# Kernel optimization log

Hardware: AMD Instinct MI355X
Metric: run time of the kernel (lower is better)

The kernel has to match this reference:

```python
import jax, jax.numpy as jnp
import numpy as np

D_MODEL = 512
NUM_HEADS = 8
PROJ_DIM = 64
SEQ_LEN = 2048
BATCH = 16
CHUNK = (SEQ_LEN + PROJ_DIM - 1) // PROJ_DIM  # 32
FILTER_HEIGHTS = (1, 3, 5)


def build_cluster_table(S, P):
    """table[R-1, c, :] = indices of positions assigned to cluster c when R real tokens, padded with R."""
    C = (S + P - 1) // P
    table = np.zeros((S, P, C), dtype=np.int32)
    cs = np.arange(P)
    for R in range(1, S + 1):
        assign = np.minimum(np.arange(R) * P // R, P - 1)  # nondecreasing
        starts = np.searchsorted(assign, cs, side='left')
        ends = np.searchsorted(assign, cs, side='right')
        row = np.full((P, C), R, dtype=np.int32)
        for c in range(P):
            n = ends[c] - starts[c]
            row[c, :n] = np.arange(starts[c], ends[c], dtype=np.int32)
        table[R - 1] = row
    return table


def setup_inputs() -> dict:
    key = jax.random.key(0)
    ks = jax.random.split(key, 16)
    glorot = lambda k, shape: jax.random.normal(k, shape, jnp.float32) * np.sqrt(2.0 / (shape[-2] + shape[-1]))
    inp = {
        'x': jax.random.normal(ks[0], (BATCH, SEQ_LEN, D_MODEL), jnp.float32),
        'mask': jnp.ones((BATCH, SEQ_LEN), dtype=bool),
        'wq': glorot(ks[1], (D_MODEL, D_MODEL)),
        'wk': glorot(ks[2], (D_MODEL, D_MODEL)),
        'wv': glorot(ks[3], (D_MODEL, D_MODEL)),
        'EW': glorot(ks[4], (NUM_HEADS, PROJ_DIM, CHUNK)),
        'FW': glorot(ks[5], (NUM_HEADS, PROJ_DIM, CHUNK)),
        'conv_w1': jax.random.normal(ks[6], (1, PROJ_DIM, 1, 1), jnp.float32) * 0.05,
        'conv_w3': jax.random.normal(ks[7], (3, PROJ_DIM, 1, 1), jnp.float32) * 0.05,
        'conv_w5': jax.random.normal(ks[8], (5, PROJ_DIM, 1, 1), jnp.float32) * 0.05,
        'conv_b': jnp.zeros((3,), jnp.float32),
        'dense_w': glorot(ks[9], (D_MODEL, D_MODEL)),
        'dense_b': jnp.zeros((D_MODEL,), jnp.float32),
        'cluster_table': jnp.asarray(build_cluster_table(SEQ_LEN, PROJ_DIM)),
    }
    return inp


def _conv_same(x, w):
    # x: [N, S, P, 1] NHWC ; w: [h, P, 1, 1] HWIO ; 'SAME' padding, stride 1
    return jax.lax.conv_general_dilated(
        x, w, window_strides=(1, 1), padding='SAME',
        dimension_numbers=('NHWC', 'HWIO', 'NHWC'))


def reference(x, mask, wq, wk, wv, EW, FW, conv_w1, conv_w3, conv_w5, conv_b,
              dense_w, dense_b, cluster_table):
    B, S, D = x.shape
    H, P, C = EW.shape
    depth = D // H

    q = x @ wq
    k = x @ wk
    v = x @ wv
    split = lambda t: t.reshape(B, S, H, depth).transpose(0, 2, 1, 3)  # [B,H,S,d]
    q, k0, v0 = split(q), split(k), split(v)

    # pad one extra (zero) position at index S for padded cluster slots
    kp = jnp.pad(k0, ((0, 0), (0, 0), (0, 1), (0, 0)))
    vp = jnp.pad(v0, ((0, 0), (0, 0), (0, 1), (0, 0)))

    counts = jnp.clip(mask.astype(jnp.int32).sum(axis=1), 1, S)
    pos = cluster_table[counts - 1]  # [B, P, C] int32

    # per-batch gather of K/V cluster chunks: [B,H,P,C,d]
    gather = lambda kv_b, pos_b: kv_b[:, pos_b, :]
    k_chunks = jax.vmap(gather)(kp, pos)
    v_chunks = jax.vmap(gather)(vp, pos)

    # clustered Linformer projections (c=proj_dim, l=chunk)
    k_proj = jnp.einsum('bhcld,hcl->bhcd', k_chunks, EW)  # [B,H,P,d]
    v_proj = jnp.einsum('bhcld,hcl->bhcd', v_chunks, FW)

    scale = 1.0 / jnp.sqrt(jnp.asarray(depth, jnp.float32))
    scores = jnp.einsum('bhsd,bhrd->bhsr', q, k_proj) * scale  # [B,H,S,P]

    # multi-kernel conv fusion over attention scores
    s4 = scores.reshape(B * H, S, P, 1)
    outs = jnp.stack([
        _conv_same(s4, conv_w1) + conv_b[0],
        _conv_same(s4, conv_w3) + conv_b[1],
        _conv_same(s4, conv_w5) + conv_b[2],
    ], axis=-1)  # [BH,S,P,1,3]
    scores = jnp.mean(outs, axis=-1)[..., 0].reshape(B, H, S, P)

    weights = jax.nn.softmax(scores, axis=-1)
    attn = jnp.einsum('bhsr,bhrd->bhsd', weights, v_proj)
    concat = attn.transpose(0, 2, 1, 3).reshape(B, S, D)
    return concat @ dense_w + dense_b
```

## Files before the change

kernel.cpp:

```cpp
#include <hip/hip_runtime.h>
#include <hip/hip_bf16.h>

typedef unsigned short u16;
typedef unsigned int   u32;
typedef unsigned char  u8;
typedef __attribute__((ext_vector_type(8))) __bf16 bfrag;
typedef __attribute__((ext_vector_type(4))) float  f32x4;

#define DEV __device__ __forceinline__

DEV u16 f2bf(float f){
  union { float f; u32 u; } v; v.f = f;
  u32 u = v.u;
  u32 r = (u + 0x7fffu + ((u >> 16) & 1u)) >> 16;
  return (u16)r;
}
DEV float bf2f(u16 x){
  union { u32 u; float f; } v; v.u = ((u32)x) << 16;
  return v.f;
}
DEV void gload16(const void* g, void* l){
  __builtin_amdgcn_global_load_lds((const __attribute__((address_space(1))) void*)g,
                                   (__attribute__((address_space(3))) void*)l, 16, 0, 0);
}

__global__ void k_prep(const float* __restrict__ x, const void* __restrict__ mask,
                       const float* __restrict__ wq, const float* __restrict__ wk,
                       const float* __restrict__ wv, const float* __restrict__ dw,
                       u16* __restrict__ xb, u16* __restrict__ wb, u16* __restrict__ dwb,
                       int* __restrict__ counts){
  int gb = blockIdx.x, t = threadIdx.x;
  if (gb < 16){
    int b = gb;
    u32 h0 = *(const u32*)mask;
    int mode = (h0 == 0x3f800000u) ? 2 : (h0 == 1u) ? 1 : 0;
    int cnt = 0;
    if (mode == 0){
      const u8* p = (const u8*)mask + (size_t)b * 2048;
      for (int i = t; i < 2048; i += 256) cnt += (p[i] != 0);
    } else if (mode == 1){
      const int* p = (const int*)mask + (size_t)b * 2048;
      for (int i = t; i < 2048; i += 256) cnt += (p[i] != 0);
    } else {
      const float* p = (const float*)mask + (size_t)b * 2048;
      for (int i = t; i < 2048; i += 256) cnt += (p[i] != 0.0f);
    }
    __shared__ int red[256];
    red[t] = cnt; __syncthreads();
    for (int s = 128; s > 0; s >>= 1){ if (t < s) red[t] += red[t + s]; __syncthreads(); }
    if (t == 0){ int c = red[0]; if (c < 1) c = 1; if (c > 2048) c = 2048; counts[b] = c; }
  } else if (gb < 400){
    int c = (gb - 16) * 256 + t;
    int kb8 = c / 1536, n = c % 1536;
    const float* w = (n < 512) ? wq : (n < 1024) ? wk : wv;
    int nn = n & 511;
    union { u16 o[8]; uint4 v; } u;
    #pragma unroll
    for (int j = 0; j < 8; ++j) u.o[j] = f2bf(w[(size_t)(kb8 * 8 + j) * 512 + nn]);
    *(uint4*)(wb + (size_t)c * 8) = u.v;
  } else if (gb < 528){
    int c = (gb - 400) * 256 + t;
    int kb8 = c >> 9, nn = c & 511;
    union { u16 o[8]; uint4 v; } u;
    #pragma unroll
    for (int j = 0; j < 8; ++j) u.o[j] = f2bf(dw[(size_t)(kb8 * 8 + j) * 512 + nn]);
    *(uint4*)(dwb + (size_t)c * 8) = u.v;
  } else {
    int i = (gb - 528) * 256 + t;
    int stride = (gridDim.x - 528) * 256;
    for (; i < 2097152; i += stride){
      const float4* s = (const float4*)(x + (size_t)i * 8);
      float4 a = s[0], b = s[1];
      union { u16 o[8]; uint4 v; } u;
      u.o[0]=f2bf(a.x); u.o[1]=f2bf(a.y); u.o[2]=f2bf(a.z); u.o[3]=f2bf(a.w);
      u.o[4]=f2bf(b.x); u.o[5]=f2bf(b.y); u.o[6]=f2bf(b.z); u.o[7]=f2bf(b.w);
      *(uint4*)(xb + (size_t)i * 8) = u.v;
    }
  }
}

template<int MODE>
__launch_bounds__(256, 8)
__global__ void k_gemm(const u16* __restrict__ A, const u16* __restrict__ Bp,
                       u16* __restrict__ q, u16* __restrict__ kk, u16* __restrict__ vv,
                       float* __restrict__ out, const float* __restrict__ bias,
                       int N, int nbn){
  __shared__ __align__(16) char sA[16384];
  __shared__ __align__(16) char sB[16384];
  const int tid = threadIdx.x;
  const int wid = tid >> 6, lane = tid & 63;
  int id = blockIdx.x;
  int per = gridDim.x >> 3;
  int lin = (id & 7) * per + (id >> 3);
  const int bm = lin / nbn;
  const int bn = lin - bm * nbn;
  const int wm = wid >> 1, wn = wid & 1;
  const int l15 = lane & 15, l4 = lane >> 4;

  f32x4 acc[4][4] = {};

  const char* Ab = (const char*)A;
  const char* Bb = (const char*)Bp;

  for (int kt = 0; kt < 8; ++kt){
    __syncthreads();
    #pragma unroll
    for (int t = 0; t < 4; ++t){
      int chunk = (wid * 4 + t) * 64 + lane;
      int row = chunk >> 3, slot = chunk & 7;
      const char* g = Ab + ((size_t)(bm * 128 + row) * 1024) + kt * 128 + ((slot ^ (row & 7)) << 4);
      gload16(g, sA + (wid * 4 + t) * 1024);
    }
    #pragma unroll
    for (int t = 0; t < 4; ++t){
      int idx = wid * 4 + t;
      int kb8l = idx >> 1, col = ((idx & 1) << 6) + lane;
      const char* g = Bb + ((size_t)((kt * 8 + kb8l) * N + bn * 128 + col) << 4);
      gload16(g, sB + idx * 1024);
    }
    __syncthreads();
    #pragma unroll
    for (int ks = 0; ks < 2; ++ks){
      bfrag af[4], bfv[4];
      #pragma unroll
      for (int mt = 0; mt < 4; ++mt){
        int row = wm * 64 + mt * 16 + l15;
        int slot = ks * 4 + l4;
        af[mt] = __builtin_bit_cast(bfrag, *(const uint4*)(sA + row * 128 + ((slot << 4) ^ ((row & 7) << 4))));
      }
      #pragma unroll
      for (int nt = 0; nt < 4; ++nt){
        int kb8l = ks * 4 + l4;
        int col = wn * 64 + nt * 16 + l15;
        bfv[nt] = __builtin_bit_cast(bfrag, *(const uint4*)(sB + ((kb8l * 128 + col) << 4)));
      }
      #pragma unroll
      for (int mt = 0; mt < 4; ++mt)
        #pragma unroll
        for (int nt = 0; nt < 4; ++nt)
          acc[mt][nt] = __builtin_amdgcn_mfma_f32_16x16x32_bf16(af[mt], bfv[nt], acc[mt][nt], 0, 0, 0);
    }
  }
  #pragma unroll
  for (int mt = 0; mt < 4; ++mt){
    #pragma unroll
    for (int nt = 0; nt < 4; ++nt){
      int col = bn * 128 + wn * 64 + nt * 16 + l15;
      #pragma unroll
      for (int r = 0; r < 4; ++r){
        int row = bm * 128 + wm * 64 + mt * 16 + (l4 << 2) + r;
        float val = acc[mt][nt][r];
        if (MODE == 0){
          int which = col >> 9, h = (col >> 6) & 7, dd = col & 63;
          u16* dst = (which == 0) ? q : (which == 1) ? kk : vv;
          int b = row >> 11, s = row & 2047;
          dst[(((size_t)(b * 8 + h) * 2048 + s) << 6) + dd] = f2bf(val);
        } else {
          out[(size_t)row * 512 + col] = val + bias[col];
        }
      }
    }
  }
}

__launch_bounds__(256, 2)
__global__ void k_proj(const u16* __restrict__ kg, const u16* __restrict__ vg,
                       const float* __restrict__ EW, const float* __restrict__ FW,
                       const float* __restrict__ w1, const float* __restrict__ w3,
                       const float* __restrict__ w5, const int* __restrict__ table,
                       const int* __restrict__ counts,
                       u16* __restrict__ KW, u16* __restrict__ vp){
  int bh = blockIdx.y, b = bh >> 3, h = bh & 7;
  int ddq = blockIdx.x;
  int t = threadIdx.x;
  __shared__ float Wf[5][128];
  __shared__ float kp[64][20];
  for (int w = t; w < 640; w += 256){
    int i = w >> 7, j = w & 127;
    float a = 0.f;
    if (j >= 32 && j < 96){
      int jj = j - 32;
      a = w5[i * 64 + jj];
      if (i >= 1 && i <= 3) a += w3[(i - 1) * 64 + jj];
      if (i == 2) a += w1[jj];
      a *= (1.0f / 3.0f) * 0.125f;
    }
    Wf[i][j] = a;
  }
  int cnt = counts[b];
  const int* tab = table + (size_t)(cnt - 1) * 2048;
  int c = t >> 2, sub = t & 3;
  int dd = ddq * 16 + sub * 4;
  float ka[4] = {0.f, 0.f, 0.f, 0.f}, va[4] = {0.f, 0.f, 0.f, 0.f};
  const u16* kbase = kg + ((size_t)bh << 17) + dd;
  const u16* vbase = vg + ((size_t)bh << 17) + dd;
  const float* ewr = EW + h * 2048 + c * 32;
  const float* fwr = FW + h * 2048 + c * 32;
  #pragma unroll
  for (int l0 = 0; l0 < 32; l0 += 8){
    int4 i0 = *(const int4*)(tab + c * 32 + l0);
    int4 i1 = *(const int4*)(tab + c * 32 + l0 + 4);
    int idx[8] = {i0.x, i0.y, i0.z, i0.w, i1.x, i1.y, i1.z, i1.w};
    uint2 kq[8], vq[8];
    #pragma unroll
    for (int j = 0; j < 8; ++j){
      int ic = idx[j] < 2047 ? idx[j] : 2047;
      kq[j] = *(const uint2*)(kbase + ((size_t)ic << 6));
      vq[j] = *(const uint2*)(vbase + ((size_t)ic << 6));
    }
    #pragma unroll
    for (int j = 0; j < 8; ++j){
      float valid = (idx[j] < 2048) ? 1.0f : 0.0f;
      float we = ewr[l0 + j] * valid, wf = fwr[l0 + j] * valid;
      union { uint2 u2; u16 s[4]; } ku, vu;
      ku.u2 = kq[j]; vu.u2 = vq[j];
      #pragma unroll
      for (int m = 0; m < 4; ++m){
        ka[m] += we * bf2f(ku.s[m]);
        va[m] += wf * bf2f(vu.s[m]);
      }
    }
  }
  *(float4*)(&kp[c][sub * 4]) = make_float4(ka[0], ka[1], ka[2], ka[3]);
  {
    int pg = c >> 3, pp = c & 7;
    #pragma unroll
    for (int m = 0; m < 4; ++m)
      vp[(((size_t)bh * 8 + pg) * 64 + (dd + m)) * 8 + pp] = f2bf(va[m]);
  }
  __syncthreads();
  float acc[5][4];
  #pragma unroll
  for (int i = 0; i < 5; ++i)
    #pragma unroll
    for (int m = 0; m < 4; ++m) acc[i][m] = 0.f;
  for (int u = 0; u < 64; ++u){
    float4 k4 = *(const float4*)(&kp[u][sub * 4]);
    #pragma unroll
    for (int i = 0; i < 5; ++i){
      float w = Wf[i][u - c + 63];
      acc[i][0] += w * k4.x; acc[i][1] += w * k4.y;
      acc[i][2] += w * k4.z; acc[i][3] += w * k4.w;
    }
  }
  #pragma unroll
  for (int i = 0; i < 5; ++i){
    union { u16 s[4]; uint2 u2; } o;
    #pragma unroll
    for (int m = 0; m < 4; ++m) o.s[m] = f2bf(acc[i][m]);
    *(uint2*)(KW + (((size_t)bh * 40 + i * 8 + (dd >> 3)) * 64 + c) * 8 + (dd & 7)) = o.u2;
  }
}

__launch_bounds__(256, 2)
__global__ void k_attn(const u16* __restrict__ qg, const u16* __restrict__ KWg,
                       const u16* __restrict__ vpg, u16* __restrict__ concat){
  __shared__ __align__(16) char sKW[40960];
  __shared__ __align__(16) char sVP[8192];
  __shared__ __align__(16) char sQ[8704];
  char* sW = sQ;
  int bh = blockIdx.y, b = bh >> 3, h = bh & 7;
  int tid = threadIdx.x, wid = tid >> 6, lane = tid & 63;
  int l15 = lane & 15, l4 = lane >> 4;

  const char* kwb = (const char*)KWg + (size_t)bh * 40960;
  #pragma unroll
  for (int t = 0; t < 10; ++t){
    int inst = wid * 10 + t;
    gload16(kwb + ((size_t)(inst * 64 + lane) << 4), sKW + inst * 1024);
  }
  const char* vpb = (const char*)vpg + (size_t)bh * 8192;
  #pragma unroll
  for (int t = 0; t < 2; ++t){
    int inst = wid * 2 + t;
    gload16(vpb + ((size_t)(inst * 64 + lane) << 4), sVP + inst * 1024);
  }
  const u16* qb = qg + ((size_t)bh << 17);

  for (int st = 0; st < 8; ++st){
    int s0 = ((blockIdx.x << 3) + st) << 6;
    for (int ch = tid; ch < 544; ch += 256){
      int row = ch >> 3, slot = ch & 7;
      int gr = s0 - 2 + row;
      uint4 val = make_uint4(0u, 0u, 0u, 0u);
      if (gr >= 0 && gr < 2048) val = *(const uint4*)(qb + ((size_t)gr << 6) + (slot << 3));
      *(uint4*)(sQ + row * 128 + ((slot << 4) ^ ((row & 7) << 4))) = val;
    }
    __syncthreads();

    f32x4 acc[4] = {};
    #pragma unroll
    for (int kb = 0; kb < 10; ++kb){
      int i = kb >> 1;
      int row = wid * 16 + l15 + i;
      int dd0b = ((kb & 1) << 6) + (l4 << 4);
      bfrag a = __builtin_bit_cast(bfrag, *(const uint4*)(sQ + row * 128 + (dd0b ^ ((row & 7) << 4))));
      int kb8 = kb * 4 + l4;
      #pragma unroll
      for (int nt = 0; nt < 4; ++nt){
        bfrag bv = __builtin_bit_cast(bfrag, *(const uint4*)(sKW + ((kb8 * 64 + nt * 16 + l15) << 4)));
        acc[nt] = __builtin_amdgcn_mfma_f32_16x16x32_bf16(a, bv, acc[nt], 0, 0, 0);
      }
    }
    float wgt[4][4];
    #pragma unroll
    for (int r = 0; r < 4; ++r){
      float m = fmaxf(fmaxf(acc[0][r], acc[1][r]), fmaxf(acc[2][r], acc[3][r]));
      m = fmaxf(m, __shfl_xor(m, 1));
      m = fmaxf(m, __shfl_xor(m, 2));
      m = fmaxf(m, __shfl_xor(m, 4));
      m = fmaxf(m, __shfl_xor(m, 8));
      float e0 = __expf(acc[0][r] - m), e1 = __expf(acc[1][r] - m);
      float e2 = __expf(acc[2][r] - m), e3 = __expf(acc[3][r] - m);
      float sum = e0 + e1 + e2 + e3;
      sum += __shfl_xor(sum, 1);
      sum += __shfl_xor(sum, 2);
      sum += __shfl_xor(sum, 4);
      sum += __shfl_xor(sum, 8);
      float inv = 1.0f / sum;
      wgt[0][r] = e0 * inv; wgt[1][r] = e1 * inv; wgt[2][r] = e2 * inv; wgt[3][r] = e3 * inv;
    }
    __syncthreads();
    #pragma unroll
    for (int r = 0; r < 4; ++r){
      int row = wid * 16 + (l4 << 2) + r;
      #pragma unroll
      for (int nt = 0; nt < 4; ++nt){
        int pb = (nt * 16 + l15) << 1;
        *(u16*)(sW + row * 128 + (pb ^ ((row & 7) << 4))) = f2bf(wgt[nt][r]);
      }
    }
    __syncthreads();
    f32x4 acc2[4] = {};
    #pragma unroll
    for (int ks = 0; ks < 2; ++ks){
      int row = wid * 16 + l15;
      int pb = (ks << 6) + (l4 << 4);
      bfrag a = __builtin_bit_cast(bfrag, *(const uint4*)(sW + row * 128 + (pb ^ ((row & 7) << 4))));
      int pg = ks * 4 + l4;
      #pragma unroll
      for (int nt = 0; nt < 4; ++nt){
        bfrag bv = __builtin_bit_cast(bfrag, *(const uint4*)(sVP + ((pg * 64 + nt * 16 + l15) << 4)));
        acc2[nt] = __builtin_amdgcn_mfma_f32_16x16x32_bf16(a, bv, acc2[nt], 0, 0, 0);
      }
    }
    #pragma unroll
    for (int nt = 0; nt < 4; ++nt){
      int col = (h << 6) + nt * 16 + l15;
      #pragma unroll
      for (int r = 0; r < 4; ++r){
        int s = s0 + wid * 16 + (l4 << 2) + r;
        concat[(((size_t)b << 11) + s) * 512 + col] = f2bf(acc2[nt][r]);
      }
    }
    __syncthreads();
  }
}

extern "C" void kernel_launch(void* const* d_in, const int* in_sizes, int n_in,
                              void* d_out, int out_size, void* d_ws, size_t ws_size,
                              hipStream_t stream){
  const float* x   = (const float*)d_in[0];
  const void*  mask= d_in[1];
  const float* wq  = (const float*)d_in[2];
  const float* wk  = (const float*)d_in[3];
  const float* wv  = (const float*)d_in[4];
  const float* EW  = (const float*)d_in[5];
  const float* FW  = (const float*)d_in[6];
  const float* cw1 = (const float*)d_in[7];
  const float* cw3 = (const float*)d_in[8];
  const float* cw5 = (const float*)d_in[9];
  const float* dw  = (const float*)d_in[11];
  const float* db  = (const float*)d_in[12];
  const int* table = (const int*)d_in[13];
  float* out = (float*)d_out;

  char* ws = (char*)d_ws;
  u16* xb     = (u16*)(ws);
  u16* wb     = (u16*)(ws + 33554432);
  u16* dwb    = (u16*)(ws + 35127296);
  u16* q      = (u16*)(ws + 35651584);
  u16* kk     = (u16*)(ws + 69206016);
  u16* vv     = (u16*)(ws + 102760448);
  u16* KW     = (u16*)(ws + 136314880);
  u16* vp     = (u16*)(ws + 141557760);
  int* counts = (int*)(ws + 142606336);
  u16* concat = xb;

  hipLaunchKernelGGL(k_prep, dim3(2064), dim3(256), 0, stream,
                     x, mask, wq, wk, wv, dw, xb, wb, dwb, counts);
  hipLaunchKernelGGL((k_gemm<0>), dim3(3072), dim3(256), 0, stream,
                     xb, wb, q, kk, vv, (float*)nullptr, (const float*)nullptr, 1536, 12);
  hipLaunchKernelGGL(k_proj, dim3(4, 128), dim3(256), 0, stream,
                     kk, vv, EW, FW, cw1, cw3, cw5, table, counts, KW, vp);
  hipLaunchKernelGGL(k_attn, dim3(4, 128), dim3(256), 0, stream, q, KW, vp, concat);
  hipLaunchKernelGGL((k_gemm<1>), dim3(1024), dim3(256), 0, stream,
                     concat, dwb, (u16*)nullptr, (u16*)nullptr, (u16*)nullptr, out, db, 512, 4);
}
```

Baseline: 183.3 us.

## Double-buffer Q tiles in attention kernel to prefetch next tile during compute

Splits the Q shared buffer into two ping-pong buffers plus a separate softmax-weight buffer, so the global loads for the next 64-row Q tile are issued into registers before the score MFMAs and stored to LDS after softmax. The load latency of the next tile can then hide behind the current tile's compute, and two of the four barriers per iteration are removed. The cost is more LDS per block (about 75 KB against about 57 KB before) and extra registers for the prefetched data, which could lower occupancy under the two-blocks-per-CU launch bound.

```diff
diff --git a/kernel.cpp b/kernel.cpp
--- a/kernel.cpp
+++ b/kernel.cpp
@@ -257,8 +257,9 @@
                        const u16* __restrict__ vpg, u16* __restrict__ concat){
   __shared__ __align__(16) char sKW[40960];
   __shared__ __align__(16) char sVP[8192];
-  __shared__ __align__(16) char sQ[8704];
-  char* sW = sQ;
+  __shared__ __align__(16) char sQ0[8704];
+  __shared__ __align__(16) char sQ1[8704];
+  __shared__ __align__(16) char sW[8704];
   int bh = blockIdx.y, b = bh >> 3, h = bh & 7;
   int tid = threadIdx.x, wid = tid >> 6, lane = tid & 63;
   int l15 = lane & 15, l4 = lane >> 4;
@@ -277,16 +278,37 @@
   }
   const u16* qb = qg + ((size_t)bh << 17);
 
-  for (int st = 0; st < 8; ++st){
-    int s0 = ((blockIdx.x << 3) + st) << 6;
+  {
+    int s0 = (blockIdx.x << 3) << 6;
     for (int ch = tid; ch < 544; ch += 256){
       int row = ch >> 3, slot = ch & 7;
       int gr = s0 - 2 + row;
       uint4 val = make_uint4(0u, 0u, 0u, 0u);
       if (gr >= 0 && gr < 2048) val = *(const uint4*)(qb + ((size_t)gr << 6) + (slot << 3));
-      *(uint4*)(sQ + row * 128 + ((slot << 4) ^ ((row & 7) << 4))) = val;
-    }
+      *(uint4*)(sQ0 + row * 128 + ((slot << 4) ^ ((row & 7) << 4))) = val;
+    }
+  }
+
+  for (int st = 0; st < 8; ++st){
+    char* cur = (st & 1) ? sQ1 : sQ0;
+    char* nxt = (st & 1) ? sQ0 : sQ1;
+    int s0 = ((blockIdx.x << 3) + st) << 6;
     __syncthreads();
+
+    uint4 qr[3];
+    if (st < 7){
+      int s0n = s0 + 64;
+      #pragma unroll
+      for (int c2 = 0; c2 < 3; ++c2){
+        int ch = tid + c2 * 256;
+        qr[c2] = make_uint4(0u, 0u, 0u, 0u);
+        if (ch < 544){
+          int row = ch >> 3, slot = ch & 7;
+          int gr = s0n - 2 + row;
+          if (gr >= 0 && gr < 2048) qr[c2] = *(const uint4*)(qb + ((size_t)gr << 6) + (slot << 3));
+        }
+      }
+    }
 
     f32x4 acc[4] = {};
     #pragma unroll
@@ -294,7 +316,7 @@
       int i = kb >> 1;
       int row = wid * 16 + l15 + i;
       int dd0b = ((kb & 1) << 6) + (l4 << 4);
-      bfrag a = __builtin_bit_cast(bfrag, *(const uint4*)(sQ + row * 128 + (dd0b ^ ((row & 7) << 4))));
+      bfrag a = __builtin_bit_cast(bfrag, *(const uint4*)(cur + row * 128 + (dd0b ^ ((row & 7) << 4))));
       int kb8 = kb * 4 + l4;
       #pragma unroll
       for (int nt = 0; nt < 4; ++nt){
@@ -320,7 +342,6 @@
       float inv = 1.0f / sum;
       wgt[0][r] = e0 * inv; wgt[1][r] = e1 * inv; wgt[2][r] = e2 * inv; wgt[3][r] = e3 * inv;
     }
-    __syncthreads();
     #pragma unroll
     for (int r = 0; r < 4; ++r){
       int row = wid * 16 + (l4 << 2) + r;
@@ -328,6 +349,16 @@
       for (int nt = 0; nt < 4; ++nt){
         int pb = (nt * 16 + l15) << 1;
         *(u16*)(sW + row * 128 + (pb ^ ((row & 7) << 4))) = f2bf(wgt[nt][r]);
+      }
+    }
+    if (st < 7){
+      #pragma unroll
+      for (int c2 = 0; c2 < 3; ++c2){
+        int ch = tid + c2 * 256;
+        if (ch < 544){
+          int row = ch >> 3, slot = ch & 7;
+          *(uint4*)(nxt + row * 128 + ((slot << 4) ^ ((row & 7) << 4))) = qr[c2];
+        }
       }
     }
     __syncthreads();
@@ -353,7 +384,6 @@
         concat[(((size_t)b << 11) + s) * 512 + col] = f2bf(acc2[nt][r]);
       }
     }
-    __syncthreads();
   }
 }
 
```

Result: no change. 180.7 us (-1.4%).
